# Kernel tuning notes

Measured on AMD Instinct MI355X. Metric: run time of the kernel, lower is better.

The kernel has to match this reference:

```python
import jax, jax.numpy as jnp
import numpy as np

T, B, F = 160, 640, 40          # time-major input [T, B, F]
H, PJ, L = 768, 256, 3          # nb_hidden, nb_proj, nb_layers
FORGET_BIAS = 1.0               # TF LSTMCell default


def _glorot(k, shape):
    std = (2.0 / (shape[0] + shape[1])) ** 0.5
    return jax.random.normal(k, shape, jnp.float32) * std


def setup_inputs() -> dict:
    key = jax.random.key(0)
    ks = jax.random.split(key, 7)
    x = jax.random.normal(ks[0], (T, B, F), jnp.float32)
    # layer 0: input dim F + proj state PJ; layers 1,2: input dim PJ + PJ
    W0 = _glorot(ks[1], (F + PJ, 4 * H)); b0 = jnp.zeros((4 * H,), jnp.float32)
    P0 = _glorot(ks[2], (H, PJ))
    W1 = _glorot(ks[3], (PJ + PJ, 4 * H)); b1 = jnp.zeros((4 * H,), jnp.float32)
    P1 = _glorot(ks[4], (H, PJ))
    W2 = _glorot(ks[5], (PJ + PJ, 4 * H)); b2 = jnp.zeros((4 * H,), jnp.float32)
    P2 = _glorot(ks[6], (H, PJ))
    return {"x": x, "W0": W0, "b0": b0, "P0": P0,
            "W1": W1, "b1": b1, "P1": P1,
            "W2": W2, "b2": b2, "P2": P2}


def _cell(xt, c, h, W, b, P):
    # TF LSTMCell with num_proj: gates on [x, m_prev]; gate order i, j, f, o.
    z = jnp.concatenate([xt, h], axis=-1) @ W + b            # [B, 4H]
    i, j, f, o = jnp.split(z, 4, axis=-1)
    c_new = jax.nn.sigmoid(f + FORGET_BIAS) * c + jax.nn.sigmoid(i) * jnp.tanh(j)
    m = jax.nn.sigmoid(o) * jnp.tanh(c_new)                  # [B, H]
    h_new = m @ P                                            # projected state [B, PJ]
    return c_new, h_new


def reference(x, W0, b0, P0, W1, b1, P1, W2, b2, P2):
    params = ((W0, b0, P0), (W1, b1, P1), (W2, b2, P2))
    Bd = x.shape[1]
    init = tuple((jnp.zeros((Bd, H), x.dtype), jnp.zeros((Bd, PJ), x.dtype))
                 for _ in range(L))

    def step(carry, xt):
        inp = xt
        new = []
        for (c, h), (W, b, P) in zip(carry, params):
            c, h = _cell(inp, c, h, W, b, P)
            new.append((c, h))
            inp = h
        return tuple(new), None

    carry, _ = jax.lax.scan(step, init, x)
    emb = carry[-1][1]                                       # last layer h at final step, [B, PJ]
    # tf.nn.l2_normalize
    return emb / jnp.sqrt(jnp.maximum(jnp.sum(emb * emb, axis=-1, keepdims=True), 1e-12))
```

## Files before the change

kernel.cpp:

```cpp
#include <hip/hip_runtime.h>

#define Bdim 640
#define Hdim 768
#define PJdim 256
#define Tdim 160
#define NSTEP (Tdim + 2)

typedef _Float16 half8 __attribute__((ext_vector_type(8)));
typedef float floatx4 __attribute__((ext_vector_type(4)));

constexpr size_t HB_HALFS = 3ull * Bdim * PJdim;
constexpr size_t ZP_OFF   = HB_HALFS * 2;
constexpr size_t MB_OFF   = ZP_OFF + 256;
constexpr size_t MB_HALFS = 3ull * Bdim * Hdim;
constexpr size_t X_OFF    = MB_OFF + MB_HALFS * 2;
constexpr size_t X_HALFS  = (size_t)Tdim * Bdim * 40;
constexpr size_t W_OFF    = X_OFF + X_HALFS * 2;
constexpr size_t W_HALFS  = 36ull * 131072;
constexpr size_t P_OFF    = W_OFF + W_HALFS * 2;
constexpr size_t P_HALFS  = 3ull * 196608;
constexpr size_t C_OFF    = P_OFF + P_HALFS * 2;
constexpr size_t C_BYTES  = 3ull * Bdim * Hdim * 4;

__device__ __forceinline__ float sigm(float v) { return 1.0f / (1.0f + __expf(-v)); }
__device__ __forceinline__ float tanh_fast(float v) { return 2.0f / (1.0f + __expf(-2.0f * v)) - 1.0f; }

__device__ __forceinline__ void stage16(void* lds, const void* g)
{
    __builtin_amdgcn_global_load_lds(
        (const __attribute__((address_space(1))) void*)g,
        (__attribute__((address_space(3))) void*)lds,
        16, 0, 0);
}
__device__ __forceinline__ void wait_vm0() {
    asm volatile("s_waitcnt vmcnt(0)" ::: "memory");
}

__device__ __forceinline__ void st_coh16b(void* p, _Float16 h) {
    union { _Float16 h; unsigned short u; } cv; cv.h = h;
    __hip_atomic_store((unsigned short*)p, cv.u, __ATOMIC_RELAXED, __HIP_MEMORY_SCOPE_AGENT);
}

__device__ __forceinline__ void pipe_wait(unsigned* c0, unsigned t0, unsigned* c1, unsigned t1)
{
    if (threadIdx.x == 0) {
        if (t0)
            while (__hip_atomic_load(c0, __ATOMIC_RELAXED, __HIP_MEMORY_SCOPE_AGENT) < t0)
                __builtin_amdgcn_s_sleep(1);
        if (c1 && t1)
            while (__hip_atomic_load(c1, __ATOMIC_RELAXED, __HIP_MEMORY_SCOPE_AGENT) < t1)
                __builtin_amdgcn_s_sleep(1);
        __builtin_amdgcn_fence(__ATOMIC_ACQUIRE, "agent");
    }
    __syncthreads();
}

__device__ __forceinline__ void pipe_sig(unsigned* c)
{
    __syncthreads();
    if (threadIdx.x == 0)
        __hip_atomic_fetch_add(c, 1u, __ATOMIC_RELAXED, __HIP_MEMORY_SCOPE_AGENT);
}

__global__ void repack_kernel(const float* __restrict__ x,
                              const float* __restrict__ W0, const float* __restrict__ W1,
                              const float* __restrict__ W2, const float* __restrict__ P0,
                              const float* __restrict__ P1, const float* __restrict__ P2,
                              _Float16* __restrict__ Wfrag, _Float16* __restrict__ Pfrag,
                              _Float16* __restrict__ x16)
{
    size_t idx = (size_t)blockIdx.x * 256 + threadIdx.x;
    if (idx < W_HALFS) {
        int slab = (int)(idx >> 17);
        int l = slab / 12, ht = slab % 12;
        int r  = (int)(idx & 131071);
        int kc = r >> 13;
        int r2 = r & 8191;
        int g  = r2 >> 11;
        int cf = (r2 >> 9) & 3;
        int u  = r2 & 511;
        int lane = u >> 3, e = u & 7;
        int qd = lane >> 4, ln = lane & 15;
        int k   = kc * 32 + qd * 8 + e;
        int col = g * Hdim + ht * 64 + cf * 16 + ln;
        float v;
        if (l == 0)      v = (k < 296) ? W0[(size_t)k * 3072 + col] : 0.0f;
        else if (l == 1) v = W1[(size_t)k * 3072 + col];
        else             v = W2[(size_t)k * 3072 + col];
        Wfrag[idx] = (_Float16)v;
    } else if (idx < W_HALFS + P_HALFS) {
        size_t i = idx - W_HALFS;
        int l = (int)(i / 196608);
        int r = (int)(i % 196608);
        int cq = r / 49152;
        int r2 = r % 49152;
        int kc = r2 / 2048;
        int r3 = r2 & 2047;
        int cgr = r3 >> 9;
        int u  = r3 & 511;
        int lane = u >> 3, e = u & 7;
        int qd = lane >> 4, ln = lane & 15;
        int k  = kc * 32 + qd * 8 + e;
        int pj = cq * 64 + cgr * 16 + ln;
        const float* P = (l == 0) ? P0 : (l == 1) ? P1 : P2;
        Pfrag[i] = (_Float16)P[(size_t)k * PJdim + pj];
    } else if (idx < W_HALFS + P_HALFS + X_HALFS) {
        size_t i = idx - W_HALFS - P_HALFS;
        x16[i] = (_Float16)x[i];
    }
}

__device__ __forceinline__ void gate_step(
    int l, int b0r, int h0, int KC, int t,
    const half8 (&Breg)[16][2], float (&c)[2][8],
    const _Float16* __restrict__ x16, const _Float16* __restrict__ h16,
    const _Float16* __restrict__ zerop, _Float16* __restrict__ mbuf,
    _Float16* __restrict__ Ast, float* __restrict__ zstA, float* __restrict__ zstB,
    const float* __restrict__ bst, int tid)
{
    const int wv = tid >> 6, lane = tid & 63, qd = lane >> 4, ln = lane & 15;
    const int g = wv >> 1, hh = wv & 1;
    const int qd8 = qd * 8;
    const int rowg = b0r + wv * 16 + ln;

    const _Float16* xt  = x16 + ((size_t)t * Bdim + rowg) * 40;
    const _Float16* h0b = h16 + (size_t)rowg * PJdim - 40;
    const _Float16* lob = (l > 0) ? h16 + ((size_t)(l - 1) * Bdim + rowg) * PJdim : nullptr;
    const _Float16* hib = h16 + ((size_t)l * Bdim + rowg) * PJdim - 256;

    auto srcp = [&](int kc) -> const _Float16* {
        int k = kc * 32 + qd8;
        if (l == 0) return (k < 40) ? xt + k : (k < 296) ? h0b + k : zerop;
        return (k < 256) ? lob + k : hib + k;
    };

    _Float16* wbase = Ast + wv * 512;
#pragma unroll
    for (int kc = 0; kc < 16; ++kc)
        if (kc < KC) stage16(wbase + (size_t)kc * 4096, srcp(kc));
    wait_vm0();
    __syncthreads();

    floatx4 acc[8][2];
    const floatx4 fz = {0.f, 0.f, 0.f, 0.f};
#pragma unroll
    for (int i = 0; i < 8; ++i) { acc[i][0] = fz; acc[i][1] = fz; }

#pragma unroll
    for (int kc = 0; kc < 16; ++kc)
        if (kc < KC) {
            const _Float16* Ab = Ast + (size_t)kc * 4096;
#pragma unroll
            for (int rf = 0; rf < 8; ++rf) {
                half8 af = *(const half8*)(Ab + rf * 512 + lane * 8);
                acc[rf][0] = __builtin_amdgcn_mfma_f32_16x16x32_f16(af, Breg[kc][0], acc[rf][0], 0, 0, 0);
                acc[rf][1] = __builtin_amdgcn_mfma_f32_16x16x32_f16(af, Breg[kc][1], acc[rf][1], 0, 0, 0);
            }
        }
    __syncthreads();

#pragma unroll
    for (int p = 0; p < 2; ++p) {
        float* zp = p ? zstB : zstA;
#pragma unroll
        for (int rq = 0; rq < 4; ++rq)
#pragma unroll
            for (int cf = 0; cf < 2; ++cf)
#pragma unroll
                for (int r = 0; r < 4; ++r)
                    zp[(rq * 16 + qd * 4 + r) * 256 + g * 64 + hh * 32 + cf * 16 + ln]
                        = acc[p * 4 + rq][cf][r];
    }
    __syncthreads();

    const int trow = tid >> 3, hcb = (tid & 7) * 8;
#pragma unroll
    for (int p = 0; p < 2; ++p) {
        const float* zrow = (p ? zstB : zstA) + trow * 256;
        union { _Float16 h[8]; uint4 v; } pk;
#pragma unroll
        for (int q = 0; q < 2; ++q) {
            const int o = q * 4;
            float4 zi = *(const float4*)(zrow + hcb + o);
            float4 zj = *(const float4*)(zrow + 64 + hcb + o);
            float4 zf = *(const float4*)(zrow + 128 + hcb + o);
            float4 zo = *(const float4*)(zrow + 192 + hcb + o);
            float4 bi = *(const float4*)(bst + hcb + o);
            float4 bj = *(const float4*)(bst + 64 + hcb + o);
            float4 bf = *(const float4*)(bst + 128 + hcb + o);
            float4 bo = *(const float4*)(bst + 192 + hcb + o);
            float cn0 = sigm(zf.x + bf.x) * c[p][o + 0] + sigm(zi.x + bi.x) * tanh_fast(zj.x + bj.x);
            float cn1 = sigm(zf.y + bf.y) * c[p][o + 1] + sigm(zi.y + bi.y) * tanh_fast(zj.y + bj.y);
            float cn2 = sigm(zf.z + bf.z) * c[p][o + 2] + sigm(zi.z + bi.z) * tanh_fast(zj.z + bj.z);
            float cn3 = sigm(zf.w + bf.w) * c[p][o + 3] + sigm(zi.w + bi.w) * tanh_fast(zj.w + bj.w);
            c[p][o + 0] = cn0; c[p][o + 1] = cn1; c[p][o + 2] = cn2; c[p][o + 3] = cn3;
            pk.h[o + 0] = (_Float16)(sigm(zo.x + bo.x) * tanh_fast(cn0));
            pk.h[o + 1] = (_Float16)(sigm(zo.y + bo.y) * tanh_fast(cn1));
            pk.h[o + 2] = (_Float16)(sigm(zo.z + bo.z) * tanh_fast(cn2));
            pk.h[o + 3] = (_Float16)(sigm(zo.w + bo.w) * tanh_fast(cn3));
        }
        *(uint4*)(mbuf + ((size_t)l * Bdim + b0r + p * 64 + trow) * Hdim + h0 + hcb) = pk.v;
    }
}

__device__ __forceinline__ void proj_step(
    int l, int b0r, int cq, const half8 (&Preg)[24],
    const _Float16* __restrict__ mbuf, _Float16* __restrict__ h16,
    _Float16* __restrict__ AstA, _Float16* __restrict__ AstB, int tid, bool xstore)
{
    const int wv = tid >> 6, lane = tid & 63, qd = lane >> 4, ln = lane & 15;
    const int rh = wv >> 2, cgi = wv & 3;
    const int rowg = b0r + wv * 16 + ln;
    const _Float16* mrow = mbuf + ((size_t)l * Bdim + rowg) * Hdim + qd * 8;
    _Float16* wA = AstA + wv * 512;
    _Float16* wB = AstB + wv * 512;

    floatx4 pacc[4];
    const floatx4 fz = {0.f, 0.f, 0.f, 0.f};
#pragma unroll
    for (int i = 0; i < 4; ++i) pacc[i] = fz;

    auto mm = [&](const _Float16* region, int base) {
#pragma unroll
        for (int kk = 0; kk < 8; ++kk) {
            const _Float16* Ab = region + (size_t)kk * 4096;
#pragma unroll
            for (int rfl = 0; rfl < 4; ++rfl) {
                half8 af = *(const half8*)(Ab + (rh * 4 + rfl) * 512 + lane * 8);
                pacc[rfl] = __builtin_amdgcn_mfma_f32_16x16x32_f16(af, Preg[base + kk], pacc[rfl], 0, 0, 0);
            }
        }
    };

#pragma unroll
    for (int kk = 0; kk < 8; ++kk) stage16(wA + (size_t)kk * 4096, mrow + kk * 32);
    wait_vm0();
    __syncthreads();
#pragma unroll
    for (int kk = 0; kk < 8; ++kk) stage16(wB + (size_t)kk * 4096, mrow + (8 + kk) * 32);
    mm(AstA, 0);
    wait_vm0();
    __syncthreads();
#pragma unroll
    for (int kk = 0; kk < 8; ++kk) stage16(wA + (size_t)kk * 4096, mrow + (16 + kk) * 32);
    mm(AstB, 8);
    wait_vm0();
    __syncthreads();
    mm(AstA, 16);

    if (xstore) {
#pragma unroll
        for (int rfl = 0; rfl < 4; ++rfl)
#pragma unroll
            for (int r = 0; r < 4; ++r) {
                int row = b0r + (rh * 4 + rfl) * 16 + qd * 4 + r;
                st_coh16b(h16 + ((size_t)l * Bdim + row) * PJdim + cq * 64 + cgi * 16 + ln,
                          (_Float16)pacc[rfl][r]);
            }
    } else {
#pragma unroll
        for (int rfl = 0; rfl < 4; ++rfl)
#pragma unroll
            for (int r = 0; r < 4; ++r) {
                int row = b0r + (rh * 4 + rfl) * 16 + qd * 4 + r;
                h16[((size_t)l * Bdim + row) * PJdim + cq * 64 + cgi * 16 + ln] = (_Float16)pacc[rfl][r];
            }
    }
}

__device__ __forceinline__ void load_Breg(const _Float16* __restrict__ Wfrag, int l, int ht,
                                          int wv, int lane, half8 (&Breg)[16][2])
{
    const int g = wv >> 1, hh = wv & 1;
    const _Float16* wslab = Wfrag + ((size_t)(l * 12 + ht)) * 131072;
#pragma unroll
    for (int kc = 0; kc < 16; ++kc)
#pragma unroll
        for (int cf = 0; cf < 2; ++cf)
            Breg[kc][cf] = *(const half8*)(wslab + kc * 8192 + g * 2048 + (hh * 2 + cf) * 512 + lane * 8);
}

__device__ __forceinline__ void load_Preg(const _Float16* __restrict__ Pfrag, int l, int cq,
                                          int wv, int lane, half8 (&Preg)[24])
{
    const int cgi = wv & 3;
    const _Float16* pslab = Pfrag + (size_t)l * 196608 + (size_t)cq * 49152;
#pragma unroll
    for (int kc = 0; kc < 24; ++kc)
        Preg[kc] = *(const half8*)(pslab + kc * 2048 + cgi * 512 + lane * 8);
}

__device__ __forceinline__ void load_bst(const float* __restrict__ bias, int h0, int tid,
                                         float* __restrict__ bst)
{
    if (tid < 256) {
        int gg = tid >> 6, u = tid & 63;
        bst[tid] = bias[gg * Hdim + h0 + u] + ((gg == 2) ? 1.0f : 0.0f);
    }
}

__device__ __forceinline__ void finalize_row(const _Float16* __restrict__ h16,
                                             float* __restrict__ out, int row, int lane)
{
    const _Float16* e = h16 + ((size_t)2 * Bdim + row) * PJdim + lane * 4;
    float v0 = (float)e[0], v1 = (float)e[1], v2 = (float)e[2], v3 = (float)e[3];
    float ss = v0 * v0 + v1 * v1 + v2 * v2 + v3 * v3;
#pragma unroll
    for (int o = 32; o > 0; o >>= 1) ss += __shfl_xor(ss, o, 64);
    float rs = rsqrtf(fmaxf(ss, 1e-12f));
    float4 o4; o4.x = v0 * rs; o4.y = v1 * rs; o4.z = v2 * rs; o4.w = v3 * rs;
    *(float4*)(out + (size_t)row * PJdim + lane * 4) = o4;
}

__global__ __launch_bounds__(512)
void lstm_persist(const _Float16* __restrict__ x16, const _Float16* __restrict__ Wfrag,
                  const _Float16* __restrict__ Pfrag,
                  const float* __restrict__ bias0, const float* __restrict__ bias1,
                  const float* __restrict__ bias2,
                  _Float16* __restrict__ h16, _Float16* __restrict__ mbuf,
                  const _Float16* __restrict__ zerop, float* __restrict__ out,
                  unsigned* __restrict__ flags)
{
    __shared__ __align__(16) char LDSRAW[132096];
    _Float16* Ast  = (_Float16*)LDSRAW;
    float*    zstA = (float*)LDSRAW;
    float*    zstB = (float*)(LDSRAW + 65536);
    float*    bst  = (float*)(LDSRAW + 131072);

    const int tid = threadIdx.x, bid = blockIdx.x;
    const int wv = tid >> 6, lane = tid & 63;

    const int xcd = bid & 7, slot = bid >> 3;
    const int gid = xcd * 2 + (slot >> 4);
    const int rr  = slot & 15;
    if (gid >= 15) return;
    const int bt2 = gid / 3, l = gid % 3;
    const int b0r = bt2 * 128;

    unsigned* gd = flags + (size_t)gid * 64;
    unsigned* pd = gd + 32;

    if (rr < 12) {
        const int ht = rr, h0 = ht * 64;
        const int KC = (l == 0) ? 10 : 16;
        half8 Breg[16][2];
        load_Breg(Wfrag, l, ht, wv, lane, Breg);
        load_bst((l == 0) ? bias0 : (l == 1) ? bias1 : bias2, h0, tid, bst);
        float c[2][8];
#pragma unroll
        for (int p = 0; p < 2; ++p)
#pragma unroll
            for (int u = 0; u < 8; ++u) c[p][u] = 0.f;
        unsigned* pd_lo = (l > 0) ? flags + (size_t)(gid - 1) * 64 + 32 : nullptr;
        for (int t = 0; t < Tdim; ++t) {
            pipe_wait(pd, 4u * (unsigned)t, pd_lo, (l > 0) ? 4u * (unsigned)(t + 1) : 0u);
            gate_step(l, b0r, h0, KC, t, Breg, c,
                      x16, h16, zerop, mbuf, Ast, zstA, zstB, bst, tid);
            pipe_sig(gd);
        }
        if (l == 2 && rr < 8) {
            pipe_wait(pd, 4u * (unsigned)Tdim, nullptr, 0u);
            int row0 = b0r + rr * 16 + wv * 2;
            finalize_row(h16, out, row0, lane);
            finalize_row(h16, out, row0 + 1, lane);
        }
    } else {
        const int cq = rr - 12;
        const bool xstore = ((gid & 1) == 1) && (gid + 1 < 15) && ((gid + 1) % 3 != 0);
        half8 Preg[24];
        load_Preg(Pfrag, l, cq, wv, lane, Preg);
        unsigned* gd_hi = (l < 2) ? flags + (size_t)(gid + 1) * 64 : nullptr;
        for (int t = 0; t < Tdim; ++t) {
            pipe_wait(gd, 12u * (unsigned)(t + 1), gd_hi, (l < 2) ? 12u * (unsigned)t : 0u);
            proj_step(l, b0r, cq, Preg, mbuf, h16, Ast, (_Float16*)(LDSRAW + 65536), tid, xstore);
            pipe_sig(pd);
        }
    }
}

__global__ __launch_bounds__(512)
void gate_fb(const _Float16* __restrict__ x16, const _Float16* __restrict__ Wfrag,
             const float* __restrict__ bias0, const float* __restrict__ bias1,
             const float* __restrict__ bias2,
             _Float16* __restrict__ h16, _Float16* __restrict__ mbuf,
             const _Float16* __restrict__ zerop, float* __restrict__ cfb, int s)
{
    __shared__ __align__(16) char LDSRAW[132096];
    _Float16* Ast  = (_Float16*)LDSRAW;
    float*    zstA = (float*)LDSRAW;
    float*    zstB = (float*)(LDSRAW + 65536);
    float*    bst  = (float*)(LDSRAW + 131072);
    const int tid = threadIdx.x, bid = blockIdx.x;
    const int ht = bid % 12, z = bid / 12, l = z % 3, bt2 = z / 3;
    const int t = s - l;
    if (t < 0 || t >= Tdim) return;
    const int wv = tid >> 6, lane = tid & 63;
    const int b0r = bt2 * 128, h0 = ht * 64;
    const int KC = (l == 0) ? 10 : 16;
    half8 Breg[16][2];
    load_Breg(Wfrag, l, ht, wv, lane, Breg);
    load_bst((l == 0) ? bias0 : (l == 1) ? bias1 : bias2, h0, tid, bst);
    __syncthreads();
    const int trow = tid >> 3, hcb = (tid & 7) * 8;
    float c[2][8];
#pragma unroll
    for (int p = 0; p < 2; ++p)
#pragma unroll
        for (int u = 0; u < 8; ++u)
            c[p][u] = cfb[((size_t)l * Bdim + b0r + p * 64 + trow) * Hdim + h0 + hcb + u];
    gate_step(l, b0r, h0, KC, t, Breg, c, x16, h16, zerop, mbuf, Ast, zstA, zstB, bst, tid);
#pragma unroll
    for (int p = 0; p < 2; ++p)
#pragma unroll
        for (int u = 0; u < 8; ++u)
            cfb[((size_t)l * Bdim + b0r + p * 64 + trow) * Hdim + h0 + hcb + u] = c[p][u];
}

__global__ __launch_bounds__(512)
void proj_fb(const _Float16* __restrict__ Pfrag, const _Float16* __restrict__ mbuf,
             _Float16* __restrict__ h16, int s)
{
    __shared__ __align__(16) char LDSRAW[131072];
    const int tid = threadIdx.x, bid = blockIdx.x;
    const int cq = bid & 3, z = bid >> 2, l = z % 3, bt2 = z / 3;
    const int tp = s - l;
    if (tp < 0 || tp >= Tdim) return;
    const int wv = tid >> 6, lane = tid & 63;
    half8 Preg[24];
    load_Preg(Pfrag, l, cq, wv, lane, Preg);
    proj_step(l, bt2 * 128, cq, Preg, mbuf, h16,
              (_Float16*)LDSRAW, (_Float16*)(LDSRAW + 65536), tid, false);
}

__global__ __launch_bounds__(512)
void fin_fb(const _Float16* __restrict__ h16, float* __restrict__ out)
{
    int row = blockIdx.x * 8 + (threadIdx.x >> 6);
    finalize_row(h16, out, row, threadIdx.x & 63);
}

extern "C" void kernel_launch(void* const* d_in, const int* in_sizes, int n_in,
                              void* d_out, int out_size, void* d_ws, size_t ws_size,
                              hipStream_t stream)
{
    (void)in_sizes; (void)n_in; (void)out_size; (void)ws_size;
    const float* x  = (const float*)d_in[0];
    const float* W0 = (const float*)d_in[1];
    const float* b0 = (const float*)d_in[2];
    const float* P0 = (const float*)d_in[3];
    const float* W1 = (const float*)d_in[4];
    const float* b1 = (const float*)d_in[5];
    const float* P1 = (const float*)d_in[6];
    const float* W2 = (const float*)d_in[7];
    const float* b2 = (const float*)d_in[8];
    const float* P2 = (const float*)d_in[9];

    char* ws = (char*)d_ws;
    _Float16* h16   = (_Float16*)(ws);
    _Float16* zerop = (_Float16*)(ws + ZP_OFF);
    _Float16* mbuf  = (_Float16*)(ws + MB_OFF);
    _Float16* x16   = (_Float16*)(ws + X_OFF);
    _Float16* Wfrag = (_Float16*)(ws + W_OFF);
    _Float16* Pfrag = (_Float16*)(ws + P_OFF);
    float*    cfb   = (float*)(ws + C_OFF);
    unsigned* flags = (unsigned*)(ws + C_OFF);
    float*    outp  = (float*)d_out;

    hipMemsetAsync(ws, 0, ZP_OFF + 256, stream);
    hipMemsetAsync(cfb, 0, C_BYTES, stream);

    {
        constexpr size_t total = W_HALFS + P_HALFS + X_HALFS;
        int grid = (int)((total + 255) / 256);
        repack_kernel<<<grid, 256, 0, stream>>>(x, W0, W1, W2, P0, P1, P2, Wfrag, Pfrag, x16);
    }

    int occ = 0;
    hipError_t oe = hipOccupancyMaxActiveBlocksPerMultiprocessor(&occ, lstm_persist, 512, 0);
    bool coop = (oe == hipSuccess && occ >= 1);
    if (coop) {
        void* args[] = { (void*)&x16, (void*)&Wfrag, (void*)&Pfrag,
                         (void*)&b0, (void*)&b1, (void*)&b2,
                         (void*)&h16, (void*)&mbuf, (void*)&zerop, (void*)&outp,
                         (void*)&flags };
        hipError_t le = hipLaunchCooperativeKernel((const void*)lstm_persist,
                                                   dim3(256), dim3(512), args, 0, stream);
        if (le != hipSuccess) { (void)hipGetLastError(); coop = false; }
    }
    if (!coop) {
        for (int s = 0; s < NSTEP; ++s) {
            gate_fb<<<180, 512, 0, stream>>>(x16, Wfrag, b0, b1, b2, h16, mbuf, zerop, cfb, s);
            proj_fb<<<60, 512, 0, stream>>>(Pfrag, mbuf, h16, s);
        }
        fin_fb<<<80, 512, 0, stream>>>(h16, outp);
    }
}
```

Before: 5.148 ms.

## Register-staged double-buffered A loads and split gate wait to overlap recurrent half

Replaces the global_load_lds bulk staging of the gate and projection A operands with register-prefetched, double-buffered LDS chunks, so global loads for the next K chunk overlap MFMA work on the current one. In the persistent gate kernel, the single combined wait is split: the recurrent-state half of the GEMM runs as soon as its own projection flag arrives, and the block only waits on the lower layer's flag before the input half. The z staging buffer is merged into one padded array (stride 258) to reduce LDS bank conflicts, and the elementwise phase is remapped to 16 columns per thread. The cost is more __syncthreads per step and more register pressure from the prefetch registers.

Result: no change. 5.140 ms (-0.2%).

```diff
diff --git a/kernel.cpp b/kernel.cpp
--- a/kernel.cpp
+++ b/kernel.cpp
@@ -5,6 +5,7 @@
 #define PJdim 256
 #define Tdim 160
 #define NSTEP (Tdim + 2)
+#define ZS 258
 
 typedef _Float16 half8 __attribute__((ext_vector_type(8)));
 typedef float floatx4 __attribute__((ext_vector_type(4)));
@@ -25,20 +26,19 @@
 __device__ __forceinline__ float sigm(float v) { return 1.0f / (1.0f + __expf(-v)); }
 __device__ __forceinline__ float tanh_fast(float v) { return 2.0f / (1.0f + __expf(-2.0f * v)) - 1.0f; }
 
-__device__ __forceinline__ void stage16(void* lds, const void* g)
-{
-    __builtin_amdgcn_global_load_lds(
-        (const __attribute__((address_space(1))) void*)g,
-        (__attribute__((address_space(3))) void*)lds,
-        16, 0, 0);
-}
-__device__ __forceinline__ void wait_vm0() {
-    asm volatile("s_waitcnt vmcnt(0)" ::: "memory");
-}
-
 __device__ __forceinline__ void st_coh16b(void* p, _Float16 h) {
     union { _Float16 h; unsigned short u; } cv; cv.h = h;
     __hip_atomic_store((unsigned short*)p, cv.u, __ATOMIC_RELAXED, __HIP_MEMORY_SCOPE_AGENT);
+}
+
+__device__ __forceinline__ void wait1(unsigned* c, unsigned tgt)
+{
+    if (threadIdx.x == 0) {
+        while (__hip_atomic_load(c, __ATOMIC_RELAXED, __HIP_MEMORY_SCOPE_AGENT) < tgt)
+            __builtin_amdgcn_s_sleep(1);
+        __builtin_amdgcn_fence(__ATOMIC_ACQUIRE, "agent");
+    }
+    __syncthreads();
 }
 
 __device__ __forceinline__ void pipe_wait(unsigned* c0, unsigned t0, unsigned* c1, unsigned t1)
@@ -111,12 +111,12 @@
 }
 
 __device__ __forceinline__ void gate_step(
-    int l, int b0r, int h0, int KC, int t,
-    const half8 (&Breg)[16][2], float (&c)[2][8],
+    int l, int b0r, int h0, int t,
+    const half8 (&Breg)[16][2], float (&c)[16],
     const _Float16* __restrict__ x16, const _Float16* __restrict__ h16,
     const _Float16* __restrict__ zerop, _Float16* __restrict__ mbuf,
-    _Float16* __restrict__ Ast, float* __restrict__ zstA, float* __restrict__ zstB,
-    const float* __restrict__ bst, int tid)
+    _Float16* __restrict__ Ast, float* __restrict__ zst, const float* __restrict__ bst,
+    unsigned* pd, unsigned pdt, unsigned* pdlo, unsigned pdlot, int tid)
 {
     const int wv = tid >> 6, lane = tid & 63, qd = lane >> 4, ln = lane & 15;
     const int g = wv >> 1, hh = wv & 1;
@@ -134,73 +134,90 @@
         return (k < 256) ? lob + k : hib + k;
     };
 
-    _Float16* wbase = Ast + wv * 512;
-#pragma unroll
-    for (int kc = 0; kc < 16; ++kc)
-        if (kc < KC) stage16(wbase + (size_t)kc * 4096, srcp(kc));
-    wait_vm0();
-    __syncthreads();
-
     floatx4 acc[8][2];
     const floatx4 fz = {0.f, 0.f, 0.f, 0.f};
 #pragma unroll
     for (int i = 0; i < 8; ++i) { acc[i][0] = fz; acc[i][1] = fz; }
 
-#pragma unroll
-    for (int kc = 0; kc < 16; ++kc)
-        if (kc < KC) {
-            const _Float16* Ab = Ast + (size_t)kc * 4096;
-#pragma unroll
-            for (int rf = 0; rf < 8; ++rf) {
-                half8 af = *(const half8*)(Ab + rf * 512 + lane * 8);
-                acc[rf][0] = __builtin_amdgcn_mfma_f32_16x16x32_f16(af, Breg[kc][0], acc[rf][0], 0, 0, 0);
-                acc[rf][1] = __builtin_amdgcn_mfma_f32_16x16x32_f16(af, Breg[kc][1], acc[rf][1], 0, 0, 0);
+    _Float16* Aw = Ast + wv * 512 + lane * 8;
+
+    auto stage_gemm = [&](int kc0, int nkc) {
+        const int ncp = nkc >> 1;
+        uint4 p0 = *(const uint4*)srcp(kc0);
+        uint4 p1 = *(const uint4*)srcp(kc0 + 1);
+#pragma unroll
+        for (int cp = 0; cp < 5; ++cp) {
+            if (cp < ncp) {
+                const int s0 = (cp & 1) * 2;
+                *(uint4*)(Aw + (size_t)s0 * 4096)       = p0;
+                *(uint4*)(Aw + (size_t)(s0 + 1) * 4096) = p1;
+                if (cp + 1 < ncp) {
+                    p0 = *(const uint4*)srcp(kc0 + 2 * cp + 2);
+                    p1 = *(const uint4*)srcp(kc0 + 2 * cp + 3);
+                }
+                __syncthreads();
+#pragma unroll
+                for (int j = 0; j < 2; ++j) {
+                    const _Float16* Ab = Ast + (size_t)(s0 + j) * 4096;
+                    const int kc = kc0 + 2 * cp + j;
+#pragma unroll
+                    for (int rf = 0; rf < 8; ++rf) {
+                        half8 af = *(const half8*)(Ab + rf * 512 + lane * 8);
+                        acc[rf][0] = __builtin_amdgcn_mfma_f32_16x16x32_f16(af, Breg[kc][0], acc[rf][0], 0, 0, 0);
+                        acc[rf][1] = __builtin_amdgcn_mfma_f32_16x16x32_f16(af, Breg[kc][1], acc[rf][1], 0, 0, 0);
+                    }
+                }
             }
         }
+    };
+
+    if (pd) wait1(pd, pdt);
+    if (l == 0) {
+        stage_gemm(0, 10);
+    } else {
+        stage_gemm(8, 8);
+        if (pdlo) wait1(pdlo, pdlot);
+        stage_gemm(0, 8);
+    }
     __syncthreads();
 
 #pragma unroll
-    for (int p = 0; p < 2; ++p) {
-        float* zp = p ? zstB : zstA;
-#pragma unroll
-        for (int rq = 0; rq < 4; ++rq)
-#pragma unroll
-            for (int cf = 0; cf < 2; ++cf)
-#pragma unroll
-                for (int r = 0; r < 4; ++r)
-                    zp[(rq * 16 + qd * 4 + r) * 256 + g * 64 + hh * 32 + cf * 16 + ln]
-                        = acc[p * 4 + rq][cf][r];
-    }
+    for (int rf = 0; rf < 8; ++rf)
+#pragma unroll
+        for (int cf = 0; cf < 2; ++cf)
+#pragma unroll
+            for (int r = 0; r < 4; ++r)
+                zst[(size_t)(rf * 16 + qd * 4 + r) * ZS + g * 64 + hh * 32 + cf * 16 + ln]
+                    = acc[rf][cf][r];
     __syncthreads();
 
-    const int trow = tid >> 3, hcb = (tid & 7) * 8;
-#pragma unroll
-    for (int p = 0; p < 2; ++p) {
-        const float* zrow = (p ? zstB : zstA) + trow * 256;
-        union { _Float16 h[8]; uint4 v; } pk;
-#pragma unroll
-        for (int q = 0; q < 2; ++q) {
-            const int o = q * 4;
-            float4 zi = *(const float4*)(zrow + hcb + o);
-            float4 zj = *(const float4*)(zrow + 64 + hcb + o);
-            float4 zf = *(const float4*)(zrow + 128 + hcb + o);
-            float4 zo = *(const float4*)(zrow + 192 + hcb + o);
-            float4 bi = *(const float4*)(bst + hcb + o);
-            float4 bj = *(const float4*)(bst + 64 + hcb + o);
-            float4 bf = *(const float4*)(bst + 128 + hcb + o);
-            float4 bo = *(const float4*)(bst + 192 + hcb + o);
-            float cn0 = sigm(zf.x + bf.x) * c[p][o + 0] + sigm(zi.x + bi.x) * tanh_fast(zj.x + bj.x);
-            float cn1 = sigm(zf.y + bf.y) * c[p][o + 1] + sigm(zi.y + bi.y) * tanh_fast(zj.y + bj.y);
-            float cn2 = sigm(zf.z + bf.z) * c[p][o + 2] + sigm(zi.z + bi.z) * tanh_fast(zj.z + bj.z);
-            float cn3 = sigm(zf.w + bf.w) * c[p][o + 3] + sigm(zi.w + bi.w) * tanh_fast(zj.w + bj.w);
-            c[p][o + 0] = cn0; c[p][o + 1] = cn1; c[p][o + 2] = cn2; c[p][o + 3] = cn3;
-            pk.h[o + 0] = (_Float16)(sigm(zo.x + bo.x) * tanh_fast(cn0));
-            pk.h[o + 1] = (_Float16)(sigm(zo.y + bo.y) * tanh_fast(cn1));
-            pk.h[o + 2] = (_Float16)(sigm(zo.z + bo.z) * tanh_fast(cn2));
-            pk.h[o + 3] = (_Float16)(sigm(zo.w + bo.w) * tanh_fast(cn3));
-        }
-        *(uint4*)(mbuf + ((size_t)l * Bdim + b0r + p * 64 + trow) * Hdim + h0 + hcb) = pk.v;
-    }
+    const int row = tid >> 2, c0 = (tid & 3) * 16;
+    const float* zrow = zst + (size_t)row * ZS;
+    union { _Float16 h[16]; uint4 v[2]; } pk;
+#pragma unroll
+    for (int q = 0; q < 4; ++q) {
+        const int o = q * 4;
+        float4 zi = *(const float4*)(zrow + c0 + o);
+        float4 zj = *(const float4*)(zrow + 64 + c0 + o);
+        float4 zf = *(const float4*)(zrow + 128 + c0 + o);
+        float4 zo = *(const float4*)(zrow + 192 + c0 + o);
+        float4 bi = *(const float4*)(bst + c0 + o);
+        float4 bj = *(const float4*)(bst + 64 + c0 + o);
+        float4 bf = *(const float4*)(bst + 128 + c0 + o);
+        float4 bo = *(const float4*)(bst + 192 + c0 + o);
+        float cn0 = sigm(zf.x + bf.x) * c[o + 0] + sigm(zi.x + bi.x) * tanh_fast(zj.x + bj.x);
+        float cn1 = sigm(zf.y + bf.y) * c[o + 1] + sigm(zi.y + bi.y) * tanh_fast(zj.y + bj.y);
+        float cn2 = sigm(zf.z + bf.z) * c[o + 2] + sigm(zi.z + bi.z) * tanh_fast(zj.z + bj.z);
+        float cn3 = sigm(zf.w + bf.w) * c[o + 3] + sigm(zi.w + bi.w) * tanh_fast(zj.w + bj.w);
+        c[o + 0] = cn0; c[o + 1] = cn1; c[o + 2] = cn2; c[o + 3] = cn3;
+        pk.h[o + 0] = (_Float16)(sigm(zo.x + bo.x) * tanh_fast(cn0));
+        pk.h[o + 1] = (_Float16)(sigm(zo.y + bo.y) * tanh_fast(cn1));
+        pk.h[o + 2] = (_Float16)(sigm(zo.z + bo.z) * tanh_fast(cn2));
+        pk.h[o + 3] = (_Float16)(sigm(zo.w + bo.w) * tanh_fast(cn3));
+    }
+    _Float16* mb = mbuf + ((size_t)l * Bdim + b0r + row) * Hdim + h0 + c0;
+    *(uint4*)mb       = pk.v[0];
+    *(uint4*)(mb + 8) = pk.v[1];
 }
 
 __device__ __forceinline__ void proj_step(
@@ -212,41 +229,43 @@
     const int rh = wv >> 2, cgi = wv & 3;
     const int rowg = b0r + wv * 16 + ln;
     const _Float16* mrow = mbuf + ((size_t)l * Bdim + rowg) * Hdim + qd * 8;
-    _Float16* wA = AstA + wv * 512;
-    _Float16* wB = AstB + wv * 512;
+    _Float16* wA = AstA + wv * 512 + lane * 8;
+    _Float16* wB = AstB + wv * 512 + lane * 8;
 
     floatx4 pacc[4];
     const floatx4 fz = {0.f, 0.f, 0.f, 0.f};
 #pragma unroll
     for (int i = 0; i < 4; ++i) pacc[i] = fz;
 
-    auto mm = [&](const _Float16* region, int base) {
-#pragma unroll
-        for (int kk = 0; kk < 8; ++kk) {
-            const _Float16* Ab = region + (size_t)kk * 4096;
+    uint4 p0 = *(const uint4*)(mrow);
+    uint4 p1 = *(const uint4*)(mrow + 32);
+    uint4 p2 = *(const uint4*)(mrow + 64);
+    uint4 p3 = *(const uint4*)(mrow + 96);
+#pragma unroll
+    for (int ch = 0; ch < 6; ++ch) {
+        _Float16* W = (ch & 1) ? wB : wA;
+        const _Float16* R = (ch & 1) ? AstB : AstA;
+        *(uint4*)(W)                      = p0;
+        *(uint4*)(W + (size_t)1 * 4096)   = p1;
+        *(uint4*)(W + (size_t)2 * 4096)   = p2;
+        *(uint4*)(W + (size_t)3 * 4096)   = p3;
+        if (ch < 5) {
+            p0 = *(const uint4*)(mrow + (4 * ch + 4) * 32);
+            p1 = *(const uint4*)(mrow + (4 * ch + 5) * 32);
+            p2 = *(const uint4*)(mrow + (4 * ch + 6) * 32);
+            p3 = *(const uint4*)(mrow + (4 * ch + 7) * 32);
+        }
+        __syncthreads();
+#pragma unroll
+        for (int kk = 0; kk < 4; ++kk) {
+            const _Float16* Ab = R + (size_t)kk * 4096;
 #pragma unroll
             for (int rfl = 0; rfl < 4; ++rfl) {
                 half8 af = *(const half8*)(Ab + (rh * 4 + rfl) * 512 + lane * 8);
-                pacc[rfl] = __builtin_amdgcn_mfma_f32_16x16x32_f16(af, Preg[base + kk], pacc[rfl], 0, 0, 0);
+                pacc[rfl] = __builtin_amdgcn_mfma_f32_16x16x32_f16(af, Preg[ch * 4 + kk], pacc[rfl], 0, 0, 0);
             }
         }
-    };
-
-#pragma unroll
-    for (int kk = 0; kk < 8; ++kk) stage16(wA + (size_t)kk * 4096, mrow + kk * 32);
-    wait_vm0();
-    __syncthreads();
-#pragma unroll
-    for (int kk = 0; kk < 8; ++kk) stage16(wB + (size_t)kk * 4096, mrow + (8 + kk) * 32);
-    mm(AstA, 0);
-    wait_vm0();
-    __syncthreads();
-#pragma unroll
-    for (int kk = 0; kk < 8; ++kk) stage16(wA + (size_t)kk * 4096, mrow + (16 + kk) * 32);
-    mm(AstB, 8);
-    wait_vm0();
-    __syncthreads();
-    mm(AstA, 16);
+    }
 
     if (xstore) {
 #pragma unroll
@@ -321,11 +340,10 @@
                   const _Float16* __restrict__ zerop, float* __restrict__ out,
                   unsigned* __restrict__ flags)
 {
-    __shared__ __align__(16) char LDSRAW[132096];
+    __shared__ __align__(16) char LDSRAW[133120];
     _Float16* Ast  = (_Float16*)LDSRAW;
-    float*    zstA = (float*)LDSRAW;
-    float*    zstB = (float*)(LDSRAW + 65536);
-    float*    bst  = (float*)(LDSRAW + 131072);
+    float*    zst  = (float*)LDSRAW;
+    float*    bst  = (float*)(LDSRAW + 132096);
 
     const int tid = threadIdx.x, bid = blockIdx.x;
     const int wv = tid >> 6, lane = tid & 63;
@@ -342,24 +360,22 @@
 
     if (rr < 12) {
         const int ht = rr, h0 = ht * 64;
-        const int KC = (l == 0) ? 10 : 16;
         half8 Breg[16][2];
         load_Breg(Wfrag, l, ht, wv, lane, Breg);
         load_bst((l == 0) ? bias0 : (l == 1) ? bias1 : bias2, h0, tid, bst);
-        float c[2][8];
-#pragma unroll
-        for (int p = 0; p < 2; ++p)
-#pragma unroll
-            for (int u = 0; u < 8; ++u) c[p][u] = 0.f;
+        float c[16];
+#pragma unroll
+        for (int u = 0; u < 16; ++u) c[u] = 0.f;
         unsigned* pd_lo = (l > 0) ? flags + (size_t)(gid - 1) * 64 + 32 : nullptr;
         for (int t = 0; t < Tdim; ++t) {
-            pipe_wait(pd, 4u * (unsigned)t, pd_lo, (l > 0) ? 4u * (unsigned)(t + 1) : 0u);
-            gate_step(l, b0r, h0, KC, t, Breg, c,
-                      x16, h16, zerop, mbuf, Ast, zstA, zstB, bst, tid);
+            gate_step(l, b0r, h0, t, Breg, c, x16, h16, zerop, mbuf,
+                      Ast, zst, bst,
+                      pd, 4u * (unsigned)t,
+                      pd_lo, (l > 0) ? 4u * (unsigned)(t + 1) : 0u, tid);
             pipe_sig(gd);
         }
         if (l == 2 && rr < 8) {
-            pipe_wait(pd, 4u * (unsigned)Tdim, nullptr, 0u);
+            wait1(pd, 4u * (unsigned)Tdim);
             int row0 = b0r + rr * 16 + wv * 2;
             finalize_row(h16, out, row0, lane);
             finalize_row(h16, out, row0 + 1, lane);
@@ -372,7 +388,8 @@
         unsigned* gd_hi = (l < 2) ? flags + (size_t)(gid + 1) * 64 : nullptr;
         for (int t = 0; t < Tdim; ++t) {
             pipe_wait(gd, 12u * (unsigned)(t + 1), gd_hi, (l < 2) ? 12u * (unsigned)t : 0u);
-            proj_step(l, b0r, cq, Preg, mbuf, h16, Ast, (_Float16*)(LDSRAW + 65536), tid, xstore);
+            proj_step(l, b0r, cq, Preg, mbuf, h16,
+                      Ast, (_Float16*)(LDSRAW + 32768), tid, xstore);
             pipe_sig(pd);
         }
     }
@@ -385,42 +402,37 @@
              _Float16* __restrict__ h16, _Float16* __restrict__ mbuf,
              const _Float16* __restrict__ zerop, float* __restrict__ cfb, int s)
 {
-    __shared__ __align__(16) char LDSRAW[132096];
+    __shared__ __align__(16) char LDSRAW[133120];
     _Float16* Ast  = (_Float16*)LDSRAW;
-    float*    zstA = (float*)LDSRAW;
-    float*    zstB = (float*)(LDSRAW + 65536);
-    float*    bst  = (float*)(LDSRAW + 131072);
+    float*    zst  = (float*)LDSRAW;
+    float*    bst  = (float*)(LDSRAW + 132096);
     const int tid = threadIdx.x, bid = blockIdx.x;
     const int ht = bid % 12, z = bid / 12, l = z % 3, bt2 = z / 3;
     const int t = s - l;
     if (t < 0 || t >= Tdim) return;
     const int wv = tid >> 6, lane = tid & 63;
     const int b0r = bt2 * 128, h0 = ht * 64;
-    const int KC = (l == 0) ? 10 : 16;
     half8 Breg[16][2];
     load_Breg(Wfrag, l, ht, wv, lane, Breg);
     load_bst((l == 0) ? bias0 : (l == 1) ? bias1 : bias2, h0, tid, bst);
     __syncthreads();
-    const int trow = tid >> 3, hcb = (tid & 7) * 8;
-    float c[2][8];
-#pragma unroll
-    for (int p = 0; p < 2; ++p)
-#pragma unroll
-        for (int u = 0; u < 8; ++u)
-            c[p][u] = cfb[((size_t)l * Bdim + b0r + p * 64 + trow) * Hdim + h0 + hcb + u];
-    gate_step(l, b0r, h0, KC, t, Breg, c, x16, h16, zerop, mbuf, Ast, zstA, zstB, bst, tid);
-#pragma unroll
-    for (int p = 0; p < 2; ++p)
-#pragma unroll
-        for (int u = 0; u < 8; ++u)
-            cfb[((size_t)l * Bdim + b0r + p * 64 + trow) * Hdim + h0 + hcb + u] = c[p][u];
+    const int row = tid >> 2, c0 = (tid & 3) * 16;
+    float c[16];
+#pragma unroll
+    for (int u = 0; u < 16; ++u)
+        c[u] = cfb[((size_t)l * Bdim + b0r + row) * Hdim + h0 + c0 + u];
+    gate_step(l, b0r, h0, t, Breg, c, x16, h16, zerop, mbuf, Ast, zst, bst,
+              nullptr, 0u, nullptr, 0u, tid);
+#pragma unroll
+    for (int u = 0; u < 16; ++u)
+        cfb[((size_t)l * Bdim + b0r + row) * Hdim + h0 + c0 + u] = c[u];
 }
 
 __global__ __launch_bounds__(512)
 void proj_fb(const _Float16* __restrict__ Pfrag, const _Float16* __restrict__ mbuf,
              _Float16* __restrict__ h16, int s)
 {
-    __shared__ __align__(16) char LDSRAW[131072];
+    __shared__ __align__(16) char LDSRAW[65536];
     const int tid = threadIdx.x, bid = blockIdx.x;
     const int cq = bid & 3, z = bid >> 2, l = z % 3, bt2 = z / 3;
     const int tp = s - l;
@@ -429,7 +441,7 @@
     half8 Preg[24];
     load_Preg(Pfrag, l, cq, wv, lane, Preg);
     proj_step(l, bt2 * 128, cq, Preg, mbuf, h16,
-              (_Float16*)LDSRAW, (_Float16*)(LDSRAW + 65536), tid, false);
+              (_Float16*)LDSRAW, (_Float16*)(LDSRAW + 32768), tid, false);
 }
 
 __global__ __launch_bounds__(512)
```
